# Performance work log

Hardware: AMD Instinct MI355X
Metric: run time of the kernel (lower is better)

Reference implementation:

```python
import jax, jax.numpy as jnp
import numpy as np

B, NF, E, T = 16, 256, 2048, 4096  # batch, features, edges, unroll_target


def setup_inputs() -> dict:
    key = jax.random.key(0)
    k1, k2, k3 = jax.random.split(key, 3)
    features = jax.random.normal(k1, (B, NF, E), dtype=jnp.float32)
    # groups: padded per-mesh unroll matrices [B, E, T] (nonneg weights; 0 in padding)
    groups = jax.random.uniform(k2, (B, E, T), dtype=jnp.float32)
    # occurrences: per-target-edge counts, >= 1 (padding is filled with 1 in the original)
    occurrences = jax.random.uniform(k3, (B, T), dtype=jnp.float32) + 1.0
    return {"features": features, "groups": groups, "occurrences": occurrences}


def reference(features, groups, occurrences):
    # unroll_mat = groups / occurrences (broadcast over source-edge dim)
    unroll_mat = groups / occurrences[:, None, :]          # [B, E, T]
    # res = features @ unroll_mat  (the sparse bmm path computes the identical result)
    res = jnp.einsum("bfe,bet->bft", features, unroll_mat)  # [B, NF, T]
    return res
```

## Files before the change

### kernel.cpp

```cpp
#include <hip/hip_runtime.h>
#include <hip/hip_bf16.h>

typedef __attribute__((ext_vector_type(4))) float          f32x4;
typedef __attribute__((ext_vector_type(8))) short          bf16x8;
typedef __attribute__((ext_vector_type(8))) unsigned short ushort8;

#define NB_   16
#define NF_   256
#define E_    2048
#define T_    4096
#define BM_   256
#define BN_   128
#define BK_   32
#define NKT   (E_ / BK_)

__device__ __forceinline__ unsigned short f2bf(float x) {
    __hip_bfloat16 h = __float2bfloat16(x);
    return __builtin_bit_cast(unsigned short, h);
}

__device__ __forceinline__ void gload_lds16(const float* g, float* l) {
    __builtin_amdgcn_global_load_lds(
        (const __attribute__((address_space(1))) void*)g,
        (__attribute__((address_space(3))) void*)l, 16, 0, 0);
}

__global__ __launch_bounds__(512, 4)
void mesh_unpool_gemm(const float* __restrict__ features,
                      const float* __restrict__ groups,
                      const float* __restrict__ occur,
                      float* __restrict__ out)
{
    const int bid = blockIdx.x;
    const int xcd = bid & 7;
    const int s   = bid >> 3;
    const int b   = xcd * 2 + (s >> 5);
    const int n0  = (s & 31) * BN_;

    const float* __restrict__ fA = features + (size_t)b * NF_ * E_;
    const float* __restrict__ fB = groups   + (size_t)b * E_ * T_;
    const float* __restrict__ fO = occur    + (size_t)b * T_;
    float* __restrict__ fC       = out      + (size_t)b * NF_ * T_;

    __shared__ float          As[2][BM_ * BK_];
    __shared__ unsigned short Bs[2][BN_ * BK_];

    const int tid  = threadIdx.x;
    const int lane = tid & 63;
    const int wave = tid >> 6;
    const int wm   = wave >> 1;
    const int wn   = wave & 1;
    const int l15  = lane & 15;
    const int kg   = lane >> 4;
    const int sw   = (l15 >> 2) & 3;
    const int bko  = (kg ^ sw) << 3;
    const int r7   = l15 & 7;
    const int ac0  = (((2 * kg)     ^ r7) << 2);
    const int ac1  = (((2 * kg + 1) ^ r7) << 2);

    const int srow = lane >> 3;
    const int schk = (lane & 7) ^ srow;
    const float* aSrc = fA + (size_t)(wave * 32 + srow) * E_ + schk * 4;

    const int tq = tid & 31;
    const int kp = tid >> 5;
    const float* bSrc = fB + (size_t)(2 * kp) * T_ + n0 + tq * 4;
    const int bSwz = ((kp >> 2) ^ (tq & 3)) << 3;
    const int bKo  = (kp & 3) << 1;

    f32x4 br0[2], br1[2];
    f32x4 acc[4][4];
    #pragma unroll
    for (int i = 0; i < 4; ++i)
        #pragma unroll
        for (int j = 0; j < 4; ++j)
            acc[i][j] = (f32x4){0.f, 0.f, 0.f, 0.f};

    auto issueA = [&](int buf, int kt) {
        const float* src = aSrc + kt * BK_;
        #pragma unroll
        for (int j = 0; j < 4; ++j)
            gload_lds16(src + (size_t)j * 8 * E_, &As[buf][(wave * 32 + j * 8) * BK_]);
    };
    auto loadB = [&](f32x4 (&br)[2], int kt) {
        const float* src = bSrc + (size_t)kt * BK_ * T_;
        br[0] = *(const f32x4*)src;
        br[1] = *(const f32x4*)(src + T_);
    };
    auto storeB = [&](int buf, f32x4 (&br)[2]) {
        #pragma unroll
        for (int i = 0; i < 4; ++i) {
            unsigned pr = (unsigned)f2bf(br[0][i]) | ((unsigned)f2bf(br[1][i]) << 16);
            *(unsigned*)&Bs[buf][(tq * 4 + i) * BK_ + bSwz + bKo] = pr;
        }
    };
    auto compute = [&](int buf) {
        bf16x8 bfr[4];
        #pragma unroll
        for (int fn = 0; fn < 4; ++fn)
            bfr[fn] = *(const bf16x8*)&Bs[buf][(wn * 64 + fn * 16 + l15) * BK_ + bko];
        #pragma unroll
        for (int fm = 0; fm < 4; ++fm) {
            const float* ar = &As[buf][(wm * 64 + fm * 16 + l15) * BK_];
            f32x4 a0 = *(const f32x4*)(ar + ac0);
            f32x4 a1 = *(const f32x4*)(ar + ac1);
            ushort8 ap;
            #pragma unroll
            for (int e = 0; e < 4; ++e) { ap[e] = f2bf(a0[e]); ap[4 + e] = f2bf(a1[e]); }
            bf16x8 af = __builtin_bit_cast(bf16x8, ap);
            #pragma unroll
            for (int fn = 0; fn < 4; ++fn)
                acc[fm][fn] = __builtin_amdgcn_mfma_f32_16x16x32_bf16(
                    af, bfr[fn], acc[fm][fn], 0, 0, 0);
        }
    };

#define KSTEP(KT, CUR, BLD, BST, HASA, HASB2, VM2)                      \
    {                                                                   \
        if (HASA) issueA((CUR) ^ 1, (KT) + 1);                          \
        __builtin_amdgcn_sched_barrier(0);                              \
        if (HASB2) loadB(BLD, (KT) + 2);                                \
        __builtin_amdgcn_sched_barrier(0);                              \
        if (HASA) storeB((CUR) ^ 1, BST);                               \
        compute(CUR);                                                   \
        asm volatile("s_waitcnt lgkmcnt(0)" ::: "memory");              \
        if (VM2) { asm volatile("s_waitcnt vmcnt(2)" ::: "memory"); }   \
        else     { asm volatile("s_waitcnt vmcnt(0)" ::: "memory"); }   \
        __builtin_amdgcn_s_barrier();                                   \
    }

    issueA(0, 0);
    __builtin_amdgcn_sched_barrier(0);
    loadB(br0, 0);
    loadB(br1, 1);
    __builtin_amdgcn_sched_barrier(0);
    storeB(0, br0);
    asm volatile("s_waitcnt lgkmcnt(0)" ::: "memory");
    asm volatile("s_waitcnt vmcnt(2)" ::: "memory");
    __builtin_amdgcn_s_barrier();

    for (int p = 0; p < 31; ++p) {
        const int kt = 2 * p;
        KSTEP(kt,     0, br0, br1, true, true, true);
        KSTEP(kt + 1, 1, br1, br0, true, true, true);
    }
    KSTEP(62, 0, br0, br1, true, false, false);
    compute(1);
#undef KSTEP

    #pragma unroll
    for (int fn = 0; fn < 4; ++fn) {
        const int t = n0 + wn * 64 + fn * 16 + l15;
        const float ro = 1.0f / fO[t];
        #pragma unroll
        for (int fm = 0; fm < 4; ++fm) {
            const int rb = wm * 64 + fm * 16 + kg * 4;
            #pragma unroll
            for (int r = 0; r < 4; ++r)
                fC[(size_t)(rb + r) * T_ + t] = acc[fm][fn][r] * ro;
        }
    }
}

extern "C" void kernel_launch(void* const* d_in, const int* in_sizes, int n_in,
                              void* d_out, int out_size, void* d_ws, size_t ws_size,
                              hipStream_t stream) {
    const float* features = (const float*)d_in[0];
    const float* groups   = (const float*)d_in[1];
    const float* occur    = (const float*)d_in[2];
    float* outp           = (float*)d_out;

    mesh_unpool_gemm<<<dim3(512), dim3(512, 1, 1), 0, stream>>>(features, groups, occur, outp);
}
```

Measured before the change: 144.5 us.

## Widen tile to 256x256 with 1024 threads and triple-buffered A prefetch

Doubles the N tile to 256, so each workgroup has 16 waves and the grid shrinks to 256 blocks. The A (features) tiles are now triple-buffered with a two-step-ahead prefetch, and B is double-buffered through registers with a new swizzled store pattern. All of this uses 128KB of dynamic LDS. The aim is to halve the redundant reloads of features per output column and to hide global latency deeper. The cost is one block per CU with 256 blocks on 256 CUs, so there is less latency hiding from co-resident blocks and more barrier cost with 16 waves.

```diff
diff --git a/kernel.cpp b/kernel.cpp
--- a/kernel.cpp
+++ b/kernel.cpp
@@ -1,18 +1,19 @@
 #include <hip/hip_runtime.h>
 #include <hip/hip_bf16.h>
 
+typedef __attribute__((ext_vector_type(2))) float          f32x2;
 typedef __attribute__((ext_vector_type(4))) float          f32x4;
 typedef __attribute__((ext_vector_type(8))) short          bf16x8;
 typedef __attribute__((ext_vector_type(8))) unsigned short ushort8;
 
-#define NB_   16
-#define NF_   256
-#define E_    2048
-#define T_    4096
-#define BM_   256
-#define BN_   128
-#define BK_   32
-#define NKT   (E_ / BK_)
+#define NB_ 16
+#define NF_ 256
+#define E_  2048
+#define T_  4096
+#define BM_ 256
+#define BN_ 256
+#define BK_ 32
+#define NKT (E_ / BK_)
 
 __device__ __forceinline__ unsigned short f2bf(float x) {
     __hip_bfloat16 h = __float2bfloat16(x);
@@ -25,31 +26,35 @@
         (__attribute__((address_space(3))) void*)l, 16, 0, 0);
 }
 
-__global__ __launch_bounds__(512, 4)
+__global__ __launch_bounds__(1024, 4)
 void mesh_unpool_gemm(const float* __restrict__ features,
                       const float* __restrict__ groups,
                       const float* __restrict__ occur,
                       float* __restrict__ out)
 {
+    extern __shared__ char smem[];
+    float* As0 = (float*)smem;
+    float* As1 = As0 + BM_ * BK_;
+    float* As2 = As1 + BM_ * BK_;
+    unsigned short* Bs0 = (unsigned short*)(As2 + BM_ * BK_);
+    unsigned short* Bs1 = Bs0 + BN_ * BK_;
+
     const int bid = blockIdx.x;
     const int xcd = bid & 7;
     const int s   = bid >> 3;
-    const int b   = xcd * 2 + (s >> 5);
-    const int n0  = (s & 31) * BN_;
+    const int b   = xcd * 2 + (s >> 4);
+    const int n0  = (s & 15) * BN_;
 
     const float* __restrict__ fA = features + (size_t)b * NF_ * E_;
     const float* __restrict__ fB = groups   + (size_t)b * E_ * T_;
     const float* __restrict__ fO = occur    + (size_t)b * T_;
     float* __restrict__ fC       = out      + (size_t)b * NF_ * T_;
 
-    __shared__ float          As[2][BM_ * BK_];
-    __shared__ unsigned short Bs[2][BN_ * BK_];
-
     const int tid  = threadIdx.x;
     const int lane = tid & 63;
     const int wave = tid >> 6;
-    const int wm   = wave >> 1;
-    const int wn   = wave & 1;
+    const int wm   = wave >> 2;
+    const int wn   = wave & 3;
     const int l15  = lane & 15;
     const int kg   = lane >> 4;
     const int sw   = (l15 >> 2) & 3;
@@ -60,15 +65,13 @@
 
     const int srow = lane >> 3;
     const int schk = (lane & 7) ^ srow;
-    const float* aSrc = fA + (size_t)(wave * 32 + srow) * E_ + schk * 4;
-
-    const int tq = tid & 31;
-    const int kp = tid >> 5;
-    const float* bSrc = fB + (size_t)(2 * kp) * T_ + n0 + tq * 4;
-    const int bSwz = ((kp >> 2) ^ (tq & 3)) << 3;
-    const int bKo  = (kp & 3) << 1;
-
-    f32x4 br0[2], br1[2];
+    const float* aSrc = fA + (size_t)(wave * 16 + srow) * E_ + schk * 4;
+
+    const int kq = tid >> 7;
+    const int cp = tid & 127;
+    const float* bSrc = fB + (size_t)(4 * kq) * T_ + n0 + 2 * cp;
+
+    f32x2 br0[4], br1[4];
     f32x4 acc[4][4];
     #pragma unroll
     for (int i = 0; i < 4; ++i)
@@ -76,32 +79,37 @@
         for (int j = 0; j < 4; ++j)
             acc[i][j] = (f32x4){0.f, 0.f, 0.f, 0.f};
 
-    auto issueA = [&](int buf, int kt) {
+    auto issueA = [&](float* AsT, int kt) {
         const float* src = aSrc + kt * BK_;
         #pragma unroll
+        for (int j = 0; j < 2; ++j)
+            gload_lds16(src + (size_t)j * 8 * E_, &AsT[(wave * 16 + j * 8) * BK_]);
+    };
+    auto loadB = [&](f32x2 (&br)[4], int kt) {
+        const float* src = bSrc + (size_t)kt * BK_ * T_;
+        #pragma unroll
         for (int j = 0; j < 4; ++j)
-            gload_lds16(src + (size_t)j * 8 * E_, &As[buf][(wave * 32 + j * 8) * BK_]);
-    };
-    auto loadB = [&](f32x4 (&br)[2], int kt) {
-        const float* src = bSrc + (size_t)kt * BK_ * T_;
-        br[0] = *(const f32x4*)src;
-        br[1] = *(const f32x4*)(src + T_);
-    };
-    auto storeB = [&](int buf, f32x4 (&br)[2]) {
-        #pragma unroll
-        for (int i = 0; i < 4; ++i) {
-            unsigned pr = (unsigned)f2bf(br[0][i]) | ((unsigned)f2bf(br[1][i]) << 16);
-            *(unsigned*)&Bs[buf][(tq * 4 + i) * BK_ + bSwz + bKo] = pr;
+            br[j] = *(const f32x2*)(src + (size_t)j * T_);
+    };
+    auto storeB = [&](unsigned short* BsT, f32x2 (&br)[4]) {
+        #pragma unroll
+        for (int ii = 0; ii < 2; ++ii) {
+            const int i = (ii + cp) & 1;
+            const int t = 2 * cp + i;
+            unsigned p0 = (unsigned)f2bf(br[0][i]) | ((unsigned)f2bf(br[1][i]) << 16);
+            unsigned p1 = (unsigned)f2bf(br[2][i]) | ((unsigned)f2bf(br[3][i]) << 16);
+            const int off = t * BK_ + (((kq >> 1) ^ ((t >> 2) & 3)) << 3) + ((kq & 1) << 2);
+            *(uint2*)&BsT[off] = make_uint2(p0, p1);
         }
     };
-    auto compute = [&](int buf) {
+    auto compute = [&](const float* AsT, const unsigned short* BsT) {
         bf16x8 bfr[4];
         #pragma unroll
         for (int fn = 0; fn < 4; ++fn)
-            bfr[fn] = *(const bf16x8*)&Bs[buf][(wn * 64 + fn * 16 + l15) * BK_ + bko];
+            bfr[fn] = *(const bf16x8*)&BsT[(wn * 64 + fn * 16 + l15) * BK_ + bko];
         #pragma unroll
         for (int fm = 0; fm < 4; ++fm) {
-            const float* ar = &As[buf][(wm * 64 + fm * 16 + l15) * BK_];
+            const float* ar = &AsT[(wm * 64 + fm * 16 + l15) * BK_];
             f32x4 a0 = *(const f32x4*)(ar + ac0);
             f32x4 a1 = *(const f32x4*)(ar + ac1);
             ushort8 ap;
@@ -115,38 +123,54 @@
         }
     };
 
-#define KSTEP(KT, CUR, BLD, BST, HASA, HASB2, VM2)                      \
+#define STEP_FULL(KT, AC, AN, BC, BNS, BLD, BST)                        \
     {                                                                   \
-        if (HASA) issueA((CUR) ^ 1, (KT) + 1);                          \
+        loadB(BLD, (KT) + 2);                                           \
+        issueA(AN, (KT) + 2);                                           \
         __builtin_amdgcn_sched_barrier(0);                              \
-        if (HASB2) loadB(BLD, (KT) + 2);                                \
+        asm volatile("s_waitcnt vmcnt(8)" ::: "memory");                \
+        storeB(BNS, BST);                                               \
+        compute(AC, BC);                                                \
         __builtin_amdgcn_sched_barrier(0);                              \
-        if (HASA) storeB((CUR) ^ 1, BST);                               \
-        compute(CUR);                                                   \
+        asm volatile("s_waitcnt vmcnt(6)" ::: "memory");                \
         asm volatile("s_waitcnt lgkmcnt(0)" ::: "memory");              \
-        if (VM2) { asm volatile("s_waitcnt vmcnt(2)" ::: "memory"); }   \
-        else     { asm volatile("s_waitcnt vmcnt(0)" ::: "memory"); }   \
         __builtin_amdgcn_s_barrier();                                   \
     }
 
-    issueA(0, 0);
+    loadB(br0, 0);
+    issueA(As0, 0);
+    loadB(br1, 1);
+    issueA(As1, 1);
     __builtin_amdgcn_sched_barrier(0);
-    loadB(br0, 0);
-    loadB(br1, 1);
+    asm volatile("s_waitcnt vmcnt(8)" ::: "memory");
+    storeB(Bs0, br0);
     __builtin_amdgcn_sched_barrier(0);
-    storeB(0, br0);
+    asm volatile("s_waitcnt vmcnt(6)" ::: "memory");
     asm volatile("s_waitcnt lgkmcnt(0)" ::: "memory");
-    asm volatile("s_waitcnt vmcnt(2)" ::: "memory");
     __builtin_amdgcn_s_barrier();
 
-    for (int p = 0; p < 31; ++p) {
-        const int kt = 2 * p;
-        KSTEP(kt,     0, br0, br1, true, true, true);
-        KSTEP(kt + 1, 1, br1, br0, true, true, true);
-    }
-    KSTEP(62, 0, br0, br1, true, false, false);
-    compute(1);
-#undef KSTEP
+    for (int p = 0; p < 10; ++p) {
+        const int kt = p * 6;
+        STEP_FULL(kt + 0, As0, As2, Bs0, Bs1, br0, br1);
+        STEP_FULL(kt + 1, As1, As0, Bs1, Bs0, br1, br0);
+        STEP_FULL(kt + 2, As2, As1, Bs0, Bs1, br0, br1);
+        STEP_FULL(kt + 3, As0, As2, Bs1, Bs0, br1, br0);
+        STEP_FULL(kt + 4, As1, As0, Bs0, Bs1, br0, br1);
+        STEP_FULL(kt + 5, As2, As1, Bs1, Bs0, br1, br0);
+    }
+    STEP_FULL(60, As0, As2, Bs0, Bs1, br0, br1);
+    STEP_FULL(61, As1, As0, Bs1, Bs0, br1, br0);
+    {
+        asm volatile("s_waitcnt vmcnt(2)" ::: "memory");
+        storeB(Bs1, br1);
+        compute(As2, Bs0);
+        __builtin_amdgcn_sched_barrier(0);
+        asm volatile("s_waitcnt vmcnt(0)" ::: "memory");
+        asm volatile("s_waitcnt lgkmcnt(0)" ::: "memory");
+        __builtin_amdgcn_s_barrier();
+    }
+    compute(As0, Bs1);
+#undef STEP_FULL
 
     #pragma unroll
     for (int fn = 0; fn < 4; ++fn) {
@@ -170,5 +194,8 @@
     const float* occur    = (const float*)d_in[2];
     float* outp           = (float*)d_out;
 
-    mesh_unpool_gemm<<<dim3(512), dim3(512, 1, 1), 0, stream>>>(features, groups, occur, outp);
-}
+    hipFuncSetAttribute((const void*)mesh_unpool_gemm,
+                        hipFuncAttributeMaxDynamicSharedMemorySize, 131072);
+    mesh_unpool_gemm<<<dim3(256), dim3(1024, 1, 1), 131072, stream>>>(
+        features, groups, occur, outp);
+}
```

New measurement: 328.0 us. 2.27x slower.
